# Kernel optimization log

Hardware: AMD Instinct MI355X
Metric: run time of the kernel (lower is better)

Reference implementation:

```python
import jax, jax.numpy as jnp
import numpy as np

D_MODEL = 1024
NUM_HEADS = 16
HEAD_DIM = D_MODEL // NUM_HEADS
THETA = 10000.0


def _trunc_normal(key, shape, std):
    # approximate trunc_normal_(a=-3std, b=3std) by clipping
    return jnp.clip(jax.random.normal(key, shape) * std, -3 * std, 3 * std)


def setup_inputs() -> dict:
    key = jax.random.key(0)
    ks = jax.random.split(key, 6)
    B, S = 2, 2048
    x = jax.random.normal(ks[0], (B, S, D_MODEL), dtype=jnp.float32)
    token_positions = jnp.sort(
        jax.random.randint(ks[1], (B, S), 0, 2048), axis=-1
    ).astype(jnp.int64)
    std = float(np.sqrt(2.0 / (D_MODEL + D_MODEL)))
    Wq = _trunc_normal(ks[2], (D_MODEL, D_MODEL), std)
    Wk = _trunc_normal(ks[3], (D_MODEL, D_MODEL), std)
    Wv = _trunc_normal(ks[4], (D_MODEL, D_MODEL), std)
    Wo = _trunc_normal(ks[5], (D_MODEL, D_MODEL), std)
    return {"x": x, "Wq": Wq, "Wk": Wk, "Wv": Wv, "Wo": Wo,
            "token_positions": token_positions}


def _rope(x, positions):
    # x: (b, h, s, d), positions: (b, s)
    d = x.shape[-1]
    inv_freq = THETA ** (-jnp.arange(0, d, 2, dtype=jnp.float32) / d)  # (d/2,)
    angles = positions.astype(jnp.float32)[:, None, :, None] * inv_freq  # (b,1,s,d/2)
    cos, sin = jnp.cos(angles), jnp.sin(angles)
    x_even, x_odd = x[..., 0::2], x[..., 1::2]
    out_even = x_even * cos - x_odd * sin
    out_odd = x_even * sin + x_odd * cos
    # interleave back: (..., d/2, 2) -> (..., d)
    return jnp.stack([out_even, out_odd], axis=-1).reshape(x.shape)


def reference(x, Wq, Wk, Wv, Wo, token_positions):
    B, S, _ = x.shape
    H, Dh = NUM_HEADS, HEAD_DIM
    # projections: einsum '... i, o i -> ... o'
    q = jnp.einsum('bsi,oi->bso', x, Wq).reshape(B, S, H, Dh).transpose(0, 2, 1, 3)
    k = jnp.einsum('bsi,oi->bso', x, Wk).reshape(B, S, H, Dh).transpose(0, 2, 1, 3)
    v = jnp.einsum('bsi,oi->bso', x, Wv).reshape(B, S, H, Dh).transpose(0, 2, 1, 3)
    q = _rope(q, token_positions)
    k = _rope(k, token_positions)
    scores = jnp.einsum('bhqd,bhkd->bhqk', q.astype(jnp.float32),
                        k.astype(jnp.float32)) / jnp.sqrt(
        jnp.asarray(Dh, dtype=jnp.float32))
    causal = jnp.tril(jnp.ones((S, S), dtype=bool))
    scores = jnp.where(causal, scores, -jnp.inf)
    attn = jax.nn.softmax(scores, axis=-1)
    out = jnp.einsum('bhqk,bhkd->bhqd', attn, v.astype(jnp.float32)).astype(x.dtype)
    out = out.transpose(0, 2, 1, 3).reshape(B, S, H * Dh)
    return jnp.einsum('bsi,oi->bso', out, Wo)
```

## Files before the change

kernel.cpp:

```cpp
#include <hip/hip_runtime.h>
#include <hip/hip_bf16.h>

#define DMODEL 1024
#define NHEADS 16
#define HDIM   64
#define BATCH  2
#define SEQ    2048
#define XELEMS ((size_t)BATCH * SEQ * DMODEL)
#define WELEMS ((size_t)DMODEL * DMODEL)

typedef __attribute__((ext_vector_type(8))) __bf16 bf16x8;
typedef __attribute__((ext_vector_type(4))) float  f32x4;
typedef __attribute__((ext_vector_type(4))) unsigned int   u32x4;
typedef __attribute__((ext_vector_type(4))) unsigned short u16x4;
typedef __attribute__((ext_vector_type(8))) unsigned short u16x8;

typedef const __attribute__((address_space(1))) void* gas_t;
typedef __attribute__((address_space(3))) void* las_t;

static __device__ __forceinline__ unsigned short f2bf(float f) {
  return __builtin_bit_cast(unsigned short, __float2bfloat16(f));
}
static __device__ __forceinline__ float bf2f(unsigned short u) {
  return __bfloat162float(__builtin_bit_cast(__hip_bfloat16, u));
}

__global__ __launch_bounds__(64) void probe_kernel(const unsigned int* __restrict__ x,
                                                   const int* __restrict__ pos,
                                                   int* __restrict__ flags) {
  const int lane = threadIdx.x;
  int bad = 0;
#pragma unroll
  for (int i = 0; i < 32; ++i) {
    const unsigned int u = x[lane * 32 + i];
    if (((u >> 23) & 0xFFu) == 0xFFu) bad++;
  }
  int zodd = 0;
#pragma unroll
  for (int i = 0; i < 4; ++i)
    if (pos[lane * 8 + 2 * i + 1] == 0) zodd++;
#pragma unroll
  for (int s = 1; s < 64; s <<= 1) {
    bad  += __shfl_xor(bad, s);
    zodd += __shfl_xor(zodd, s);
  }
  if (lane == 0) {
    flags[0] = (bad < 64) ? 1 : 0;
    flags[1] = (zodd >= 200) ? 1 : 0;
  }
}

__global__ __launch_bounds__(256) void conv_kernel(
    const void* __restrict__ x,
    const void* __restrict__ w0, const void* __restrict__ w1,
    const void* __restrict__ w2, const void* __restrict__ w3,
    unsigned short* __restrict__ dst, const int* __restrict__ flags) {
  const size_t e = ((size_t)blockIdx.x * 256 + threadIdx.x) * 8;
  const void* src;
  size_t off;
  if (e < XELEMS) { src = x; off = e; }
  else {
    const size_t r = e - XELEMS;
    const int wi = (int)(r >> 20);
    src = (wi == 0) ? w0 : (wi == 1) ? w1 : (wi == 2) ? w2 : w3;
    off = r & (WELEMS - 1);
  }
  if (flags[0]) {
    const float* s = (const float*)src + off;
    const f32x4 a = *(const f32x4*)(s);
    const f32x4 b = *(const f32x4*)(s + 4);
    u16x8 o8;
#pragma unroll
    for (int j = 0; j < 4; ++j) o8[j] = f2bf(a[j]);
#pragma unroll
    for (int j = 0; j < 4; ++j) o8[4 + j] = f2bf(b[j]);
    *(u16x8*)(dst + e) = o8;
  } else {
    *(u32x4*)(dst + e) = *(const u32x4*)((const unsigned short*)src + off);
  }
}

__device__ __forceinline__ void gemm_core(const unsigned short* __restrict__ Ag,
                                          const unsigned short* __restrict__ Bg,
                                          unsigned short* As, unsigned short* Bs,
                                          int bm, int bn, f32x4 acc[4][4]) {
  const int tid = threadIdx.x;
  const int lane = tid & 63;
  const int w  = tid >> 6;
  const int wm = w >> 1, wn = w & 1;
  const int c = lane & 15, g = lane >> 4;
  const int r0 = tid >> 2;
  const int s0 = (tid & 3) * 8;
  for (int k0 = 0; k0 < DMODEL; k0 += 32) {
    __syncthreads();
    __builtin_amdgcn_global_load_lds((gas_t)(Ag + (size_t)(bm + r0) * DMODEL + k0 + s0),
                                     (las_t)(As + tid * 8), 16, 0, 0);
    __builtin_amdgcn_global_load_lds((gas_t)(Ag + (size_t)(bm + r0 + 64) * DMODEL + k0 + s0),
                                     (las_t)(As + (tid + 256) * 8), 16, 0, 0);
    __builtin_amdgcn_global_load_lds((gas_t)(Bg + (size_t)(bn + r0) * DMODEL + k0 + s0),
                                     (las_t)(Bs + tid * 8), 16, 0, 0);
    __builtin_amdgcn_global_load_lds((gas_t)(Bg + (size_t)(bn + r0 + 64) * DMODEL + k0 + s0),
                                     (las_t)(Bs + (tid + 256) * 8), 16, 0, 0);
    __syncthreads();
    bf16x8 af[4], bfr[4];
#pragma unroll
    for (int m = 0; m < 4; ++m)
      af[m] = *(const bf16x8*)&As[(wm * 64 + m * 16 + c) * 32 + g * 8];
#pragma unroll
    for (int n = 0; n < 4; ++n)
      bfr[n] = *(const bf16x8*)&Bs[(wn * 64 + n * 16 + c) * 32 + g * 8];
#pragma unroll
    for (int m = 0; m < 4; ++m)
#pragma unroll
      for (int n = 0; n < 4; ++n)
        acc[m][n] = __builtin_amdgcn_mfma_f32_16x16x32_bf16(af[m], bfr[n], acc[m][n], 0, 0, 0);
  }
}

__global__ __launch_bounds__(256) void qkv_gemm_kernel(
    const unsigned short* __restrict__ x,
    const unsigned short* __restrict__ Wq, const unsigned short* __restrict__ Wk,
    const unsigned short* __restrict__ Wv,
    unsigned short* __restrict__ qo, unsigned short* __restrict__ ko,
    unsigned short* __restrict__ vto) {
  __shared__ unsigned short As[128 * 32];
  __shared__ unsigned short Bs[128 * 32];
  const int z = blockIdx.z;
  const unsigned short* W = (z == 0) ? Wq : (z == 1) ? Wk : Wv;
  const int bm = blockIdx.x * 128, bn = blockIdx.y * 128;
  f32x4 acc[4][4];
#pragma unroll
  for (int m = 0; m < 4; ++m)
#pragma unroll
    for (int n = 0; n < 4; ++n)
#pragma unroll
      for (int j = 0; j < 4; ++j) acc[m][n][j] = 0.f;

  gemm_core(x, W, As, Bs, bm, bn, acc);

  const int tid = threadIdx.x, lane = tid & 63, w = tid >> 6;
  const int wm = w >> 1, wn = w & 1, c = lane & 15, g4 = lane >> 4;
#pragma unroll
  for (int m = 0; m < 4; ++m) {
#pragma unroll
    for (int n = 0; n < 4; ++n) {
      const int col = bn + wn * 64 + n * 16 + c;
      const int h = col >> 6, d = col & 63;
      const int row0 = bm + wm * 64 + m * 16 + g4 * 4;
      if (z == 2) {
        const int b = row0 >> 11, s0 = row0 & (SEQ - 1);
        u16x4 pk;
#pragma unroll
        for (int j = 0; j < 4; ++j) pk[j] = f2bf(acc[m][n][j]);
        *(u16x4*)&vto[((size_t)(b * NHEADS + h) * HDIM + d) * SEQ + s0] = pk;
      } else {
        unsigned short* dst = z ? ko : qo;
#pragma unroll
        for (int j = 0; j < 4; ++j) {
          const int row = row0 + j;
          const int b = row >> 11, s = row & (SEQ - 1);
          dst[((size_t)(b * NHEADS + h) * SEQ + s) * HDIM + d] = f2bf(acc[m][n][j]);
        }
      }
    }
  }
}

__global__ __launch_bounds__(256) void out_gemm_kernel(
    const unsigned short* __restrict__ A, const unsigned short* __restrict__ Wo,
    void* __restrict__ outv, const int* __restrict__ flags) {
  __shared__ unsigned short As[128 * 32];
  __shared__ unsigned short Bs[128 * 32];
  const int bm = blockIdx.x * 128, bn = blockIdx.y * 128;
  f32x4 acc[4][4];
#pragma unroll
  for (int m = 0; m < 4; ++m)
#pragma unroll
    for (int n = 0; n < 4; ++n)
#pragma unroll
      for (int j = 0; j < 4; ++j) acc[m][n][j] = 0.f;

  gemm_core(A, Wo, As, Bs, bm, bn, acc);

  const int tid = threadIdx.x, lane = tid & 63, w = tid >> 6;
  const int wm = w >> 1, wn = w & 1, c = lane & 15, g4 = lane >> 4;
  const int f32o = flags[0];
  if (f32o) {
    float* out = (float*)outv;
#pragma unroll
    for (int m = 0; m < 4; ++m)
#pragma unroll
      for (int n = 0; n < 4; ++n) {
        const int col = bn + wn * 64 + n * 16 + c;
#pragma unroll
        for (int j = 0; j < 4; ++j) {
          const int row = bm + wm * 64 + m * 16 + g4 * 4 + j;
          out[(size_t)row * DMODEL + col] = acc[m][n][j];
        }
      }
  } else {
    unsigned short* out = (unsigned short*)outv;
#pragma unroll
    for (int m = 0; m < 4; ++m)
#pragma unroll
      for (int n = 0; n < 4; ++n) {
        const int col = bn + wn * 64 + n * 16 + c;
#pragma unroll
        for (int j = 0; j < 4; ++j) {
          const int row = bm + wm * 64 + m * 16 + g4 * 4 + j;
          out[(size_t)row * DMODEL + col] = f2bf(acc[m][n][j]);
        }
      }
  }
}

__global__ __launch_bounds__(256) void rope_kernel(unsigned short* __restrict__ q,
                                                   unsigned short* __restrict__ k,
                                                   const int* __restrict__ pos,
                                                   const int* __restrict__ flags) {
  const int idx = blockIdx.x * 256 + threadIdx.x;
  const int tsel = idx >> 21;
  const int p = idx & ((1 << 21) - 1);
  const int j = p & 31;
  const int s = (p >> 5) & (SEQ - 1);
  const int bh = p >> 16;
  const int b = bh >> 4;
  unsigned short* base = tsel ? k : q;
  const int pidx = b * SEQ + s;
  const int pv = flags[1] ? pos[2 * pidx] : pos[pidx];
  const float sc = tsel ? 1.0f : 0.125f;
  const float freq = exp2f((float)j * -0.41524101186092026f);
  const float ang = (float)pv * freq;
  const float cs = cosf(ang);
  const float sn = sinf(ang);
  unsigned int* wp = (unsigned int*)base + ((p >> 5) * 32 + j);
  const unsigned int u = *wp;
  const float e = bf2f((unsigned short)(u & 0xffffu));
  const float o = bf2f((unsigned short)(u >> 16));
  *wp = (unsigned int)f2bf((e * cs - o * sn) * sc) |
        ((unsigned int)f2bf((e * sn + o * cs) * sc) << 16);
}

#define MNEG -1e30f
#define QBLK 64
#define LOG2E 1.4426950408889634f
__global__ __launch_bounds__(256, 4) void flash_kernel(
    const unsigned short* __restrict__ q, const unsigned short* __restrict__ k,
    const unsigned short* __restrict__ vt, unsigned short* __restrict__ o) {
  __shared__ unsigned short Ks[2][64 * 64];
  __shared__ unsigned short Vs[64 * 64];
  __shared__ unsigned short Ps[64 * 72];

  const int wg = blockIdx.x;
  const int qt = (SEQ / QBLK - 1) - (wg >> 5);
  const int bh = wg & 31;
  const int qbase = qt * QBLK;
  const int tid = threadIdx.x, lane = tid & 63, w = tid >> 6;
  const int c = lane & 15, g = lane >> 4;
  const int wq = w * 16;
  const size_t tb = (size_t)bh * SEQ * HDIM;

  bf16x8 qf[2];
#pragma unroll
  for (int kk = 0; kk < 2; ++kk)
    qf[kk] = *(const bf16x8*)(q + tb + (size_t)(qbase + wq + c) * HDIM + kk * 32 + g * 8);

#pragma unroll
  for (int i = 0; i < 2; ++i) {
    const int t = tid + i * 256;
    const int r = t >> 3;
    const int sl = (t & 7) ^ (r & 7);
    __builtin_amdgcn_global_load_lds((gas_t)(k + tb + (size_t)r * HDIM + sl * 8),
                                     (las_t)(Ks[0] + t * 8), 16, 0, 0);
  }
  __syncthreads();

  f32x4 acco[4];
#pragma unroll
  for (int n = 0; n < 4; ++n)
#pragma unroll
    for (int j = 0; j < 4; ++j) acco[n][j] = 0.f;
  float m_r = MNEG, l_r = 0.f;

  const int nkv = qt + 1;
  for (int kt = 0; kt < nkv; ++kt) {
    const int p = kt & 1;
    const int kvb = kt * 64;
#pragma unroll
    for (int i = 0; i < 2; ++i) {
      const int t = tid + i * 256;
      const int r = t >> 3;
      const int sl = (t & 7) ^ (r & 7);
      __builtin_amdgcn_global_load_lds((gas_t)(vt + tb + (size_t)r * SEQ + kvb + sl * 8),
                                       (las_t)(Vs + t * 8), 16, 0, 0);
    }
    if (kt + 1 < nkv) {
      const int kvb1 = kvb + 64;
#pragma unroll
      for (int i = 0; i < 2; ++i) {
        const int t = tid + i * 256;
        const int r = t >> 3;
        const int sl = (t & 7) ^ (r & 7);
        __builtin_amdgcn_global_load_lds((gas_t)(k + tb + (size_t)(kvb1 + r) * HDIM + sl * 8),
                                         (las_t)(Ks[p ^ 1] + t * 8), 16, 0, 0);
      }
    }

    f32x4 accs[4];
#pragma unroll
    for (int n = 0; n < 4; ++n)
#pragma unroll
      for (int j = 0; j < 4; ++j) accs[n][j] = 0.f;
#pragma unroll
    for (int kk = 0; kk < 2; ++kk)
#pragma unroll
      for (int n = 0; n < 4; ++n) {
        const int r = n * 16 + c;
        const int sl = (kk * 4 + g) ^ (r & 7);
        const bf16x8 ak = *(const bf16x8*)&Ks[p][r * 64 + sl * 8];
        accs[n] = __builtin_amdgcn_mfma_f32_16x16x32_bf16(ak, qf[kk], accs[n], 0, 0, 0);
      }

    const int qg = qbase + wq + c;
    if (kt == qt) {
#pragma unroll
      for (int n = 0; n < 4; ++n)
#pragma unroll
        for (int jj = 0; jj < 4; ++jj)
          if (kvb + n * 16 + g * 4 + jj > qg) accs[n][jj] = MNEG;
    }

    float rm = accs[0][0];
#pragma unroll
    for (int n = 0; n < 4; ++n)
#pragma unroll
      for (int jj = 0; jj < 4; ++jj) rm = fmaxf(rm, accs[n][jj]);
    rm = fmaxf(rm, __shfl_xor(rm, 16));
    rm = fmaxf(rm, __shfl_xor(rm, 32));
    const float mn = fmaxf(m_r, rm);
    const float al = exp2f((m_r - mn) * LOG2E);
    float rs = 0.f;
#pragma unroll
    for (int n = 0; n < 4; ++n)
#pragma unroll
      for (int jj = 0; jj < 4; ++jj) {
        const float pv = exp2f((accs[n][jj] - mn) * LOG2E);
        accs[n][jj] = pv;
        rs += pv;
      }
    rs += __shfl_xor(rs, 16);
    rs += __shfl_xor(rs, 32);
    l_r = l_r * al + rs;
    m_r = mn;
#pragma unroll
    for (int n = 0; n < 4; ++n)
#pragma unroll
      for (int jj = 0; jj < 4; ++jj) acco[n][jj] *= al;

#pragma unroll
    for (int n = 0; n < 4; ++n) {
      u16x4 pk4;
#pragma unroll
      for (int jj = 0; jj < 4; ++jj) pk4[jj] = f2bf(accs[n][jj]);
      *(u16x4*)&Ps[(wq + c) * 72 + n * 16 + g * 4] = pk4;
    }

    asm volatile("s_waitcnt vmcnt(0)" ::: "memory");

#pragma unroll
    for (int kk = 0; kk < 2; ++kk) {
      const bf16x8 pb = *(const bf16x8*)&Ps[(wq + c) * 72 + kk * 32 + g * 8];
#pragma unroll
      for (int n = 0; n < 4; ++n) {
        const int r = n * 16 + c;
        const int sl = (kk * 4 + g) ^ (r & 7);
        const bf16x8 av = *(const bf16x8*)&Vs[r * 64 + sl * 8];
        acco[n] = __builtin_amdgcn_mfma_f32_16x16x32_bf16(av, pb, acco[n], 0, 0, 0);
      }
    }
    __syncthreads();
  }

  const float rl = 1.f / fmaxf(l_r, 1e-20f);
  const int b = bh >> 4, h = bh & 15;
  const int srow = qbase + wq + c;
#pragma unroll
  for (int n = 0; n < 4; ++n) {
    u16x4 pk;
#pragma unroll
    for (int jj = 0; jj < 4; ++jj) pk[jj] = f2bf(acco[n][jj] * rl);
    *(u16x4*)&o[(size_t)(b * SEQ + srow) * DMODEL + h * 64 + n * 16 + g * 4] = pk;
  }
}

extern "C" void kernel_launch(void* const* d_in, const int* in_sizes, int n_in,
                              void* d_out, int out_size, void* d_ws, size_t ws_size,
                              hipStream_t stream) {
  (void)in_sizes; (void)n_in; (void)out_size; (void)ws_size;
  const size_t MB = (size_t)1 << 20;
  char* ws = (char*)d_ws;
  unsigned short* xb  = (unsigned short*)(ws);
  unsigned short* Wqb = (unsigned short*)(ws + 8 * MB);
  unsigned short* Wkb = (unsigned short*)(ws + 10 * MB);
  unsigned short* Wvb = (unsigned short*)(ws + 12 * MB);
  unsigned short* Wob = (unsigned short*)(ws + 14 * MB);
  unsigned short* qw  = (unsigned short*)(ws + 16 * MB);
  unsigned short* kw  = (unsigned short*)(ws + 24 * MB);
  unsigned short* vtw = (unsigned short*)(ws + 32 * MB);
  int* flags          = (int*)(ws + 40 * MB);
  unsigned short* ow  = xb;

  const dim3 blk(256);
  probe_kernel<<<1, 64, 0, stream>>>((const unsigned int*)d_in[0], (const int*)d_in[5], flags);
  conv_kernel<<<4096, blk, 0, stream>>>(d_in[0], d_in[1], d_in[2], d_in[3], d_in[4], xb, flags);
  qkv_gemm_kernel<<<dim3(32, 8, 3), blk, 0, stream>>>(xb, Wqb, Wkb, Wvb, qw, kw, vtw);
  rope_kernel<<<16384, blk, 0, stream>>>(qw, kw, (const int*)d_in[5], flags);
  flash_kernel<<<dim3(1024), blk, 0, stream>>>(qw, kw, vtw, ow);
  out_gemm_kernel<<<dim3(32, 8), blk, 0, stream>>>(ow, Wob, d_out, flags);
}
```

Measured before the change: 134.1 us.

## Double-buffer GEMM and flash K/V tiles, add lazy softmax rescaling

Both GEMM kernels now double-buffer their LDS A/B tiles, so the next k-slice's global-to-LDS loads overlap the current slice's MFMAs. This drops one barrier per iteration. The flash kernel double-buffers V alongside K, prefetching both one tile ahead, and removes the explicit vmcnt wait before PV. It also skips the running-max rescale unless some lane's max grows by more than a threshold. In exchange, LDS use doubles, the flash occupancy hint drops from 4 to 3, and the lazy rescale lets exponentials exceed 1 within a bounded range. Removing the vmcnt wait may be unsafe if the prefetched V is read before the async loads finish.

```diff
diff --git a/kernel.cpp b/kernel.cpp
--- a/kernel.cpp
+++ b/kernel.cpp
@@ -91,29 +91,40 @@
   const int c = lane & 15, g = lane >> 4;
   const int r0 = tid >> 2;
   const int s0 = (tid & 3) * 8;
+
+  auto stage = [&](int buf, int k0) {
+    unsigned short* ad = As + buf * 4096;
+    unsigned short* bd = Bs + buf * 4096;
+    __builtin_amdgcn_global_load_lds((gas_t)(Ag + (size_t)(bm + r0) * DMODEL + k0 + s0),
+                                     (las_t)(ad + tid * 8), 16, 0, 0);
+    __builtin_amdgcn_global_load_lds((gas_t)(Ag + (size_t)(bm + r0 + 64) * DMODEL + k0 + s0),
+                                     (las_t)(ad + (tid + 256) * 8), 16, 0, 0);
+    __builtin_amdgcn_global_load_lds((gas_t)(Bg + (size_t)(bn + r0) * DMODEL + k0 + s0),
+                                     (las_t)(bd + tid * 8), 16, 0, 0);
+    __builtin_amdgcn_global_load_lds((gas_t)(Bg + (size_t)(bn + r0 + 64) * DMODEL + k0 + s0),
+                                     (las_t)(bd + (tid + 256) * 8), 16, 0, 0);
+  };
+
+  stage(0, 0);
+  __syncthreads();
   for (int k0 = 0; k0 < DMODEL; k0 += 32) {
-    __syncthreads();
-    __builtin_amdgcn_global_load_lds((gas_t)(Ag + (size_t)(bm + r0) * DMODEL + k0 + s0),
-                                     (las_t)(As + tid * 8), 16, 0, 0);
-    __builtin_amdgcn_global_load_lds((gas_t)(Ag + (size_t)(bm + r0 + 64) * DMODEL + k0 + s0),
-                                     (las_t)(As + (tid + 256) * 8), 16, 0, 0);
-    __builtin_amdgcn_global_load_lds((gas_t)(Bg + (size_t)(bn + r0) * DMODEL + k0 + s0),
-                                     (las_t)(Bs + tid * 8), 16, 0, 0);
-    __builtin_amdgcn_global_load_lds((gas_t)(Bg + (size_t)(bn + r0 + 64) * DMODEL + k0 + s0),
-                                     (las_t)(Bs + (tid + 256) * 8), 16, 0, 0);
-    __syncthreads();
+    const int cur = (k0 >> 5) & 1;
+    if (k0 + 32 < DMODEL) stage(cur ^ 1, k0 + 32);
+    const unsigned short* ar = As + cur * 4096;
+    const unsigned short* br = Bs + cur * 4096;
     bf16x8 af[4], bfr[4];
 #pragma unroll
     for (int m = 0; m < 4; ++m)
-      af[m] = *(const bf16x8*)&As[(wm * 64 + m * 16 + c) * 32 + g * 8];
-#pragma unroll
-    for (int n = 0; n < 4; ++n)
-      bfr[n] = *(const bf16x8*)&Bs[(wn * 64 + n * 16 + c) * 32 + g * 8];
+      af[m] = *(const bf16x8*)&ar[(wm * 64 + m * 16 + c) * 32 + g * 8];
+#pragma unroll
+    for (int n = 0; n < 4; ++n)
+      bfr[n] = *(const bf16x8*)&br[(wn * 64 + n * 16 + c) * 32 + g * 8];
 #pragma unroll
     for (int m = 0; m < 4; ++m)
 #pragma unroll
       for (int n = 0; n < 4; ++n)
         acc[m][n] = __builtin_amdgcn_mfma_f32_16x16x32_bf16(af[m], bfr[n], acc[m][n], 0, 0, 0);
+    __syncthreads();
   }
 }
 
@@ -123,8 +134,8 @@
     const unsigned short* __restrict__ Wv,
     unsigned short* __restrict__ qo, unsigned short* __restrict__ ko,
     unsigned short* __restrict__ vto) {
-  __shared__ unsigned short As[128 * 32];
-  __shared__ unsigned short Bs[128 * 32];
+  __shared__ unsigned short As[2 * 128 * 32];
+  __shared__ unsigned short Bs[2 * 128 * 32];
   const int z = blockIdx.z;
   const unsigned short* W = (z == 0) ? Wq : (z == 1) ? Wk : Wv;
   const int bm = blockIdx.x * 128, bn = blockIdx.y * 128;
@@ -169,8 +180,8 @@
 __global__ __launch_bounds__(256) void out_gemm_kernel(
     const unsigned short* __restrict__ A, const unsigned short* __restrict__ Wo,
     void* __restrict__ outv, const int* __restrict__ flags) {
-  __shared__ unsigned short As[128 * 32];
-  __shared__ unsigned short Bs[128 * 32];
+  __shared__ unsigned short As[2 * 128 * 32];
+  __shared__ unsigned short Bs[2 * 128 * 32];
   const int bm = blockIdx.x * 128, bn = blockIdx.y * 128;
   f32x4 acc[4][4];
 #pragma unroll
@@ -244,11 +255,11 @@
 #define MNEG -1e30f
 #define QBLK 64
 #define LOG2E 1.4426950408889634f
-__global__ __launch_bounds__(256, 4) void flash_kernel(
+__global__ __launch_bounds__(256, 3) void flash_kernel(
     const unsigned short* __restrict__ q, const unsigned short* __restrict__ k,
     const unsigned short* __restrict__ vt, unsigned short* __restrict__ o) {
   __shared__ unsigned short Ks[2][64 * 64];
-  __shared__ unsigned short Vs[64 * 64];
+  __shared__ unsigned short Vs[2][64 * 64];
   __shared__ unsigned short Ps[64 * 72];
 
   const int wg = blockIdx.x;
@@ -265,14 +276,20 @@
   for (int kk = 0; kk < 2; ++kk)
     qf[kk] = *(const bf16x8*)(q + tb + (size_t)(qbase + wq + c) * HDIM + kk * 32 + g * 8);
 
-#pragma unroll
-  for (int i = 0; i < 2; ++i) {
-    const int t = tid + i * 256;
-    const int r = t >> 3;
-    const int sl = (t & 7) ^ (r & 7);
-    __builtin_amdgcn_global_load_lds((gas_t)(k + tb + (size_t)r * HDIM + sl * 8),
-                                     (las_t)(Ks[0] + t * 8), 16, 0, 0);
-  }
+  auto stageKV = [&](int buf, int kvb) {
+#pragma unroll
+    for (int i = 0; i < 2; ++i) {
+      const int t = tid + i * 256;
+      const int r = t >> 3;
+      const int sl = (t & 7) ^ (r & 7);
+      __builtin_amdgcn_global_load_lds((gas_t)(k + tb + (size_t)(kvb + r) * HDIM + sl * 8),
+                                       (las_t)(Ks[buf] + t * 8), 16, 0, 0);
+      __builtin_amdgcn_global_load_lds((gas_t)(vt + tb + (size_t)r * SEQ + kvb + sl * 8),
+                                       (las_t)(Vs[buf] + t * 8), 16, 0, 0);
+    }
+  };
+
+  stageKV(0, 0);
   __syncthreads();
 
   f32x4 acco[4];
@@ -286,25 +303,7 @@
   for (int kt = 0; kt < nkv; ++kt) {
     const int p = kt & 1;
     const int kvb = kt * 64;
-#pragma unroll
-    for (int i = 0; i < 2; ++i) {
-      const int t = tid + i * 256;
-      const int r = t >> 3;
-      const int sl = (t & 7) ^ (r & 7);
-      __builtin_amdgcn_global_load_lds((gas_t)(vt + tb + (size_t)r * SEQ + kvb + sl * 8),
-                                       (las_t)(Vs + t * 8), 16, 0, 0);
-    }
-    if (kt + 1 < nkv) {
-      const int kvb1 = kvb + 64;
-#pragma unroll
-      for (int i = 0; i < 2; ++i) {
-        const int t = tid + i * 256;
-        const int r = t >> 3;
-        const int sl = (t & 7) ^ (r & 7);
-        __builtin_amdgcn_global_load_lds((gas_t)(k + tb + (size_t)(kvb1 + r) * HDIM + sl * 8),
-                                         (las_t)(Ks[p ^ 1] + t * 8), 16, 0, 0);
-      }
-    }
+    if (kt + 1 < nkv) stageKV(p ^ 1, kvb + 64);
 
     f32x4 accs[4];
 #pragma unroll
@@ -337,25 +336,28 @@
       for (int jj = 0; jj < 4; ++jj) rm = fmaxf(rm, accs[n][jj]);
     rm = fmaxf(rm, __shfl_xor(rm, 16));
     rm = fmaxf(rm, __shfl_xor(rm, 32));
-    const float mn = fmaxf(m_r, rm);
-    const float al = exp2f((m_r - mn) * LOG2E);
+    if (!__all(rm <= m_r + 8.f)) {
+      const float mn = fmaxf(m_r, rm);
+      const float al = exp2f((m_r - mn) * LOG2E);
+      l_r *= al;
+#pragma unroll
+      for (int n = 0; n < 4; ++n)
+#pragma unroll
+        for (int jj = 0; jj < 4; ++jj) acco[n][jj] *= al;
+      m_r = mn;
+    }
     float rs = 0.f;
 #pragma unroll
     for (int n = 0; n < 4; ++n)
 #pragma unroll
       for (int jj = 0; jj < 4; ++jj) {
-        const float pv = exp2f((accs[n][jj] - mn) * LOG2E);
+        const float pv = exp2f((accs[n][jj] - m_r) * LOG2E);
         accs[n][jj] = pv;
         rs += pv;
       }
     rs += __shfl_xor(rs, 16);
     rs += __shfl_xor(rs, 32);
-    l_r = l_r * al + rs;
-    m_r = mn;
-#pragma unroll
-    for (int n = 0; n < 4; ++n)
-#pragma unroll
-      for (int jj = 0; jj < 4; ++jj) acco[n][jj] *= al;
+    l_r += rs;
 
 #pragma unroll
     for (int n = 0; n < 4; ++n) {
@@ -364,8 +366,6 @@
       for (int jj = 0; jj < 4; ++jj) pk4[jj] = f2bf(accs[n][jj]);
       *(u16x4*)&Ps[(wq + c) * 72 + n * 16 + g * 4] = pk4;
     }
-
-    asm volatile("s_waitcnt vmcnt(0)" ::: "memory");
 
 #pragma unroll
     for (int kk = 0; kk < 2; ++kk) {
@@ -374,7 +374,7 @@
       for (int n = 0; n < 4; ++n) {
         const int r = n * 16 + c;
         const int sl = (kk * 4 + g) ^ (r & 7);
-        const bf16x8 av = *(const bf16x8*)&Vs[r * 64 + sl * 8];
+        const bf16x8 av = *(const bf16x8*)&Vs[p][r * 64 + sl * 8];
         acco[n] = __builtin_amdgcn_mfma_f32_16x16x32_bf16(av, pb, acco[n], 0, 0, 0);
       }
     }
```

Result: no change. 134.5 us (+0.3%).
